# Optimization experiments

Hardware: AMD Instinct MI355X
Metric: run time of the kernel (lower is better)

## Reference

```python
import jax, jax.numpy as jnp
import numpy as np

EMB = 1024
HEADS = 16
HEAD_SZ = EMB // HEADS
EPS = 1e-5


def _layernorm(x, g, b):
    mu = jnp.mean(x, axis=-1, keepdims=True)
    var = jnp.mean(jnp.square(x - mu), axis=-1, keepdims=True)
    return (x - mu) * jax.lax.rsqrt(var + EPS) * g + b


def setup_inputs() -> dict:
    key = jax.random.key(0)
    ks = jax.random.split(key, 12)
    s_in = 1.0 / np.sqrt(EMB)
    s_h = 1.0 / np.sqrt(4 * EMB)
    return {
        "x": jax.random.normal(ks[0], (4, 1024, EMB), jnp.float32),
        # per-head Q/K/V projections stacked: [H, EMB, HEAD_SZ], no bias
        "wq": jax.random.normal(ks[1], (HEADS, EMB, HEAD_SZ), jnp.float32) * s_in,
        "wk": jax.random.normal(ks[2], (HEADS, EMB, HEAD_SZ), jnp.float32) * s_in,
        "wv": jax.random.normal(ks[3], (HEADS, EMB, HEAD_SZ), jnp.float32) * s_in,
        "w_proj": jax.random.normal(ks[4], (EMB, EMB), jnp.float32) * s_in,
        "b_proj": jnp.zeros((EMB,), jnp.float32),
        "w1": jax.random.normal(ks[5], (EMB, 4 * EMB), jnp.float32) * s_in,
        "b1": jnp.zeros((4 * EMB,), jnp.float32),
        "w2": jax.random.normal(ks[6], (4 * EMB, EMB), jnp.float32) * s_h,
        "b2": jnp.zeros((EMB,), jnp.float32),
        "g1": jnp.ones((EMB,), jnp.float32),
        "be1": jnp.zeros((EMB,), jnp.float32),
        "g2": jnp.ones((EMB,), jnp.float32),
        "be2": jnp.zeros((EMB,), jnp.float32),
    }


def reference(x, wq, wk, wv, w_proj, b_proj, w1, b1, w2, b2, g1, be1, g2, be2):
    B, T, C = x.shape
    # --- self-attention (pre-norm) ---
    h = _layernorm(x, g1, be1)
    q = jnp.einsum("btc,hcd->bhtd", h, wq)
    k = jnp.einsum("btc,hcd->bhtd", h, wk)
    v = jnp.einsum("btc,hcd->bhtd", h, wv)
    scale = 1.0 / jnp.sqrt(jnp.asarray(HEAD_SZ, x.dtype))
    scores = jnp.einsum("bhtd,bhsd->bhts", q, k) * scale  # non-causal: SDPA called with no mask
    attn = jax.nn.softmax(scores, axis=-1)
    o = jnp.einsum("bhts,bhsd->bhtd", attn, v)
    o = o.transpose(0, 2, 1, 3).reshape(B, T, C)  # concat heads (same order as torch.cat)
    sa_out = o @ w_proj + b_proj
    x = x + sa_out
    # --- feed-forward; note ln2 applied twice, faithful to source ---
    t = _layernorm(x, g2, be2)
    t = _layernorm(t, g2, be2)
    ff = jax.nn.relu(t @ w1 + b1) @ w2 + b2
    return x + ff
```

## Files before the change

### kernel.cpp

```cpp
#include <hip/hip_runtime.h>
#include <hip/hip_bf16.h>
#include <math.h>
#include <stdint.h>

typedef __bf16 bf16_t;
typedef __bf16 bf16x4 __attribute__((ext_vector_type(4)));
typedef __bf16 bf16x8 __attribute__((ext_vector_type(8)));
typedef float floatx4 __attribute__((ext_vector_type(4)));

#define BM 128
#define BK 32

__device__ __forceinline__ void gload16(const void* g, void* lds) {
    __builtin_amdgcn_global_load_lds(
        (__attribute__((address_space(1))) void*)(uintptr_t)g,
        (__attribute__((address_space(3))) void*)(uintptr_t)lds,
        16, 0, 0);
}

__global__ void transpose_all(const float* __restrict__ wq, const float* __restrict__ wk,
                              const float* __restrict__ wv, const float* __restrict__ w_proj,
                              const float* __restrict__ w1, const float* __restrict__ w2,
                              bf16_t* __restrict__ WQKVT, bf16_t* __restrict__ WPROJT,
                              bf16_t* __restrict__ W1T, bf16_t* __restrict__ W2T)
{
    const int idx = blockIdx.x;
    const float* in; bf16_t* out; int R, C, rt, ct; long nrow0;
    if (idx < 768) {
        const int z = idx >> 8;
        const int hd = (idx >> 4) & 15;
        rt = idx & 15; ct = 0; R = 1024; C = 64;
        in  = (z == 0 ? wq : z == 1 ? wk : wv) + hd * 65536;
        out = WQKVT; nrow0 = z * 1024 + hd * 64;
    } else if (idx < 1024) {
        const int t = idx - 768; rt = t & 15; ct = t >> 4; R = 1024; C = 1024;
        in = w_proj; out = WPROJT; nrow0 = 0;
    } else if (idx < 2048) {
        const int t = idx - 1024; rt = t & 15; ct = t >> 4; R = 1024; C = 4096;
        in = w1; out = W1T; nrow0 = 0;
    } else {
        const int t = idx - 2048; rt = t & 63; ct = t >> 6; R = 4096; C = 1024;
        in = w2; out = W2T; nrow0 = 0;
    }
    __shared__ float tile[64][65];
    const int tid = threadIdx.x;
    const int r0 = rt * 64, c0 = ct * 64;
    const int tr = tid >> 4;
    const int tc = (tid & 15) * 4;
#pragma unroll
    for (int rr = 0; rr < 4; rr++) {
        const int r = tr + rr * 16;
        const float4 v = *(const float4*)&in[(long)(r0 + r) * C + c0 + tc];
        tile[r][tc + 0] = v.x; tile[r][tc + 1] = v.y;
        tile[r][tc + 2] = v.z; tile[r][tc + 3] = v.w;
    }
    __syncthreads();
    const int KT = R >> 5;
#pragma unroll
    for (int rr = 0; rr < 4; rr++) {
        const int c = tr + rr * 16;
        const long n = nrow0 + c0 + c;
        const int k = r0 + tc;
        bf16x4 o;
        o[0] = (bf16_t)tile[tc + 0][c];
        o[1] = (bf16_t)tile[tc + 1][c];
        o[2] = (bf16_t)tile[tc + 2][c];
        o[3] = (bf16_t)tile[tc + 3][c];
        const long addr = ((n >> 4) * KT + (k >> 5)) * 512
                        + (((k >> 3) & 3) * 16 + (n & 15)) * 8 + (k & 7);
        *(bf16x4*)&out[addr] = o;
    }
}

__global__ void ln_kernel(const float* __restrict__ x, const float* __restrict__ g,
                          const float* __restrict__ b, bf16_t* __restrict__ outb)
{
    const int row = blockIdx.x;
    const int tid = threadIdx.x;
    const float4 v = ((const float4*)(x + (long)row * 1024))[tid];
    float s  = v.x + v.y + v.z + v.w;
    float s2 = v.x * v.x + v.y * v.y + v.z * v.z + v.w * v.w;
#pragma unroll
    for (int off = 32; off >= 1; off >>= 1) {
        s  += __shfl_xor(s, off);
        s2 += __shfl_xor(s2, off);
    }
    __shared__ float red[8];
    const int wv = tid >> 6;
    if ((tid & 63) == 0) { red[wv] = s; red[4 + wv] = s2; }
    __syncthreads();
    s  = red[0] + red[1] + red[2] + red[3];
    s2 = red[4] + red[5] + red[6] + red[7];
    const float mu  = s * (1.0f / 1024.0f);
    const float var = fmaxf(s2 * (1.0f / 1024.0f) - mu * mu, 0.0f);
    const float rs  = rsqrtf(var + 1e-5f);
    const float4 gv = ((const float4*)g)[tid];
    const float4 bv = ((const float4*)b)[tid];
    bf16x4 o;
    o[0] = (bf16_t)((v.x - mu) * rs * gv.x + bv.x);
    o[1] = (bf16_t)((v.y - mu) * rs * gv.y + bv.y);
    o[2] = (bf16_t)((v.z - mu) * rs * gv.z + bv.z);
    o[3] = (bf16_t)((v.w - mu) * rs * gv.w + bv.w);
    ((bf16x4*)(outb + (long)row * 1024))[tid] = o;
}

__global__ void ln2x_kernel(const float* __restrict__ x, const float* __restrict__ g,
                            const float* __restrict__ b, bf16_t* __restrict__ outb)
{
    const int row = blockIdx.x;
    const int tid = threadIdx.x;
    const float4 v = ((const float4*)(x + (long)row * 1024))[tid];
    float s  = v.x + v.y + v.z + v.w;
    float s2 = v.x * v.x + v.y * v.y + v.z * v.z + v.w * v.w;
#pragma unroll
    for (int off = 32; off >= 1; off >>= 1) {
        s  += __shfl_xor(s, off);
        s2 += __shfl_xor(s2, off);
    }
    __shared__ float red[8];
    __shared__ float red2[8];
    const int wv = tid >> 6;
    if ((tid & 63) == 0) { red[wv] = s; red[4 + wv] = s2; }
    __syncthreads();
    s  = red[0] + red[1] + red[2] + red[3];
    s2 = red[4] + red[5] + red[6] + red[7];
    float mu  = s * (1.0f / 1024.0f);
    float var = fmaxf(s2 * (1.0f / 1024.0f) - mu * mu, 0.0f);
    float rs  = rsqrtf(var + 1e-5f);
    const float4 gv = ((const float4*)g)[tid];
    const float4 bv = ((const float4*)b)[tid];
    float y0 = (v.x - mu) * rs * gv.x + bv.x;
    float y1 = (v.y - mu) * rs * gv.y + bv.y;
    float y2 = (v.z - mu) * rs * gv.z + bv.z;
    float y3 = (v.w - mu) * rs * gv.w + bv.w;
    s  = y0 + y1 + y2 + y3;
    s2 = y0 * y0 + y1 * y1 + y2 * y2 + y3 * y3;
#pragma unroll
    for (int off = 32; off >= 1; off >>= 1) {
        s  += __shfl_xor(s, off);
        s2 += __shfl_xor(s2, off);
    }
    if ((tid & 63) == 0) { red2[wv] = s; red2[4 + wv] = s2; }
    __syncthreads();
    s  = red2[0] + red2[1] + red2[2] + red2[3];
    s2 = red2[4] + red2[5] + red2[6] + red2[7];
    mu  = s * (1.0f / 1024.0f);
    var = fmaxf(s2 * (1.0f / 1024.0f) - mu * mu, 0.0f);
    rs  = rsqrtf(var + 1e-5f);
    bf16x4 o;
    o[0] = (bf16_t)((y0 - mu) * rs * gv.x + bv.x);
    o[1] = (bf16_t)((y1 - mu) * rs * gv.y + bv.y);
    o[2] = (bf16_t)((y2 - mu) * rs * gv.z + bv.z);
    o[3] = (bf16_t)((y3 - mu) * rs * gv.w + bv.w);
    ((bf16x4*)(outb + (long)row * 1024))[tid] = o;
}

template<int EPI, int BNt>
__global__ __launch_bounds__(256, 2)
void gemm_bt(const bf16_t* __restrict__ A, const bf16_t* __restrict__ Bt,
             const int K,
             const float* __restrict__ bias, const float* __restrict__ resid,
             float* __restrict__ outf, bf16_t* __restrict__ outb,
             bf16_t* __restrict__ aux1, bf16_t* __restrict__ aux2,
             const int Nout)
{
    constexpr int NFRAG = BNt / 16;
    __shared__ __align__(16) bf16_t As[3][BM * BK];
    __shared__ __align__(16) bf16_t Bs[3][NFRAG * 512];
    const int tid  = threadIdx.x;
    const int wave = tid >> 6, lane = tid & 63;
    const int bm = blockIdx.x * BM, bn = blockIdx.y * BNt;

    floatx4 acc[2][NFRAG];
#pragma unroll
    for (int i = 0; i < 2; i++)
#pragma unroll
        for (int j = 0; j < NFRAG; j++) acc[i][j] = (floatx4){0.f, 0.f, 0.f, 0.f};

    const int srow  = lane >> 2;
    const int selem = (lane & 3) * 8;
    const bf16_t* gA0 = A + (size_t)(bm + wave * 32 + srow) * K + selem;
    const bf16_t* gA1 = gA0 + (size_t)16 * K;
    const int laOff0 = (wave * 32 + srow) * BK + selem;
    const int laOff1 = laOff0 + 16 * BK;
    const int lA0 = (wave * 32) * BK;
    const int lA1 = (wave * 32 + 16) * BK;

    const int KT = K >> 5;
    const bf16_t* gB0;
    const bf16_t* gB1 = nullptr;
    int lB0, lB1 = 0;
    if (BNt == 128) {
        gB0 = Bt + ((size_t)(bn / 16 + wave * 2 + 0) * KT) * 512 + lane * 8;
        gB1 = Bt + ((size_t)(bn / 16 + wave * 2 + 1) * KT) * 512 + lane * 8;
        lB0 = (wave * 2 + 0) * 512;
        lB1 = (wave * 2 + 1) * 512;
    } else {
        gB0 = Bt + ((size_t)(bn / 16 + wave) * KT) * 512 + lane * 8;
        lB0 = wave * 512;
    }

    const int fr = lane & 15;
    const int fk = (lane >> 4) * 8;

    auto stage = [&](int t, int bu) {
        const size_t offA = (size_t)t * BK;
        const size_t offB = (size_t)t * 512;
        gload16(gA0 + offA, (bf16_t*)As[bu] + lA0);
        gload16(gA1 + offA, (bf16_t*)As[bu] + lA1);
        gload16(gB0 + offB, (bf16_t*)Bs[bu] + lB0);
        if (BNt == 128) gload16(gB1 + offB, (bf16_t*)Bs[bu] + lB1);
    };

    auto compute = [&](int bu) {
        bf16x8 af[2], bfv[NFRAG];
#pragma unroll
        for (int i = 0; i < 2; i++)
            af[i] = *(const bf16x8*)&As[bu][(wave * 32 + i * 16 + fr) * BK + fk];
#pragma unroll
        for (int j = 0; j < NFRAG; j++)
            bfv[j] = *(const bf16x8*)&Bs[bu][j * 512 + lane * 8];
#pragma unroll
        for (int i = 0; i < 2; i++)
#pragma unroll
            for (int j = 0; j < NFRAG; j++)
                acc[i][j] = __builtin_amdgcn_mfma_f32_16x16x32_bf16(af[i], bfv[j], acc[i][j], 0, 0, 0);
    };

    const int NT = K / BK;
    stage(0, 0);
    stage(1, 1);
    int bu = 0;
    for (int t = 0; t < NT - 1; ++t) {
        if (BNt == 128) asm volatile("s_waitcnt vmcnt(4)\n\ts_barrier" ::: "memory");
        else            asm volatile("s_waitcnt vmcnt(3)\n\ts_barrier" ::: "memory");
        if (t + 2 < NT) stage(t + 2, (t + 2) % 3);
        compute(bu);
        bu = (bu + 1) % 3;
    }
    asm volatile("s_waitcnt vmcnt(0)\n\ts_barrier" ::: "memory");
    compute(bu);

    const int er = (lane >> 4) * 4, ec = lane & 15;
#pragma unroll
    for (int i = 0; i < 2; i++) {
#pragma unroll
        for (int j = 0; j < NFRAG; j++) {
            const int col = bn + j * 16 + ec;
#pragma unroll
            for (int r = 0; r < 4; r++) {
                const int row = bm + wave * 32 + i * 16 + er + r;
                const float v = acc[i][j][r];
                if (EPI == 0) {
                    const int b = row >> 10, t = row & 1023;
                    if (col < 1024) {
                        const int h = col >> 6, d = col & 63;
                        outb[(size_t)((b * 16 + h) * 1024 + t) * 64 + d] = (bf16_t)v;
                    } else if (col < 2048) {
                        const int c2 = col - 1024, h = c2 >> 6, d = c2 & 63;
                        aux1[(size_t)((b * 16 + h) * 1024 + t) * 64 + d] = (bf16_t)v;
                    } else {
                        const int c2 = col - 2048, h = c2 >> 6, d = c2 & 63;
                        aux2[(size_t)((b * 16 + h) * 64 + d) * 1024 + t] = (bf16_t)v;
                    }
                } else if (EPI == 1 || EPI == 3) {
                    const size_t idx = (size_t)row * Nout + col;
                    outf[idx] = v + bias[col] + resid[idx];
                } else if (EPI == 2) {
                    const size_t idx = (size_t)row * Nout + col;
                    outb[idx] = (bf16_t)fmaxf(v + bias[col], 0.f);
                }
            }
        }
    }
}

__global__ __launch_bounds__(256, 4)
void attn_kernel(const bf16_t* __restrict__ Q, const bf16_t* __restrict__ Kg,
                 const bf16_t* __restrict__ Vt, bf16_t* __restrict__ Og)
{
    __shared__ __align__(16) bf16_t Ks[2][4096];
    __shared__ __align__(16) bf16_t Vs[2][4096];
    __shared__ __align__(16) bf16_t Ps[4][1024];
    const int tid = threadIdx.x, wave = tid >> 6, lane = tid & 63;
    const int bh = blockIdx.y;
    const int b = bh >> 4, h = bh & 15;
    const int q0 = blockIdx.x * 64 + wave * 16;
    const bf16_t* Qb = Q + (size_t)bh * 65536;
    const char* Kb = (const char*)(Kg + (size_t)bh * 65536);
    const char* Vb = (const char*)(Vt + (size_t)bh * 65536);
    const int fr = lane & 15, g = lane >> 4, fk = g * 8;

    const bf16x8 qf0 = *(const bf16x8*)&Qb[(size_t)(q0 + fr) * 64 + fk];
    const bf16x8 qf1 = *(const bf16x8*)&Qb[(size_t)(q0 + fr) * 64 + 32 + fk];

    floatx4 o[4];
#pragma unroll
    for (int dt = 0; dt < 4; dt++) o[dt] = (floatx4){0.f, 0.f, 0.f, 0.f};
    float lsum[4] = {0.f, 0.f, 0.f, 0.f};
    bf16_t* pw = &Ps[wave][0];
    const float sscale = 0.125f * 1.44269504088896f;

    auto stage = [&](int s0, int bu) {
#pragma unroll
        for (int t = 0; t < 2; t++) {
            const int j = wave * 2 + t;
            gload16(Kb + (size_t)(s0 + lane) * 128 + j * 16, &Ks[bu][j * 512]);
            gload16(Vb + (size_t)lane * 2048 + (size_t)s0 * 2 + j * 16, &Vs[bu][j * 512]);
        }
    };

    stage(0, 0);
    int bu = 0;
    for (int it = 0; it < 16; ++it) {
        __syncthreads();
        if (it < 15) stage((it + 1) * 64, bu ^ 1);
        const bf16_t* Kl = Ks[bu];
        const bf16_t* Vl = Vs[bu];

        floatx4 sacc[4];
#pragma unroll
        for (int ss = 0; ss < 4; ss++) sacc[ss] = (floatx4){0.f, 0.f, 0.f, 0.f};
#pragma unroll
        for (int c = 0; c < 2; c++) {
            const int ch = c * 4 + g;
            const bf16x8 qf = (c == 0) ? qf0 : qf1;
#pragma unroll
            for (int ss = 0; ss < 4; ss++) {
                const bf16x8 kf = *(const bf16x8*)&Kl[ch * 512 + (ss * 16 + fr) * 8];
                sacc[ss] = __builtin_amdgcn_mfma_f32_16x16x32_bf16(qf, kf, sacc[ss], 0, 0, 0);
            }
        }
#pragma unroll
        for (int ss = 0; ss < 4; ss++) {
#pragma unroll
            for (int r = 0; r < 4; r++) {
                const float p = __builtin_amdgcn_exp2f(sacc[ss][r] * sscale);
                lsum[r] += p;
                const int q = g * 4 + r;
                pw[(ss * 2 + (fr >> 3)) * 128 + q * 8 + (fr & 7)] = (bf16_t)p;
            }
        }
        asm volatile("s_waitcnt lgkmcnt(0)" ::: "memory");
#pragma unroll
        for (int c = 0; c < 2; c++) {
            const int ch = c * 4 + g;
            const bf16x8 pf = *(const bf16x8*)&pw[ch * 128 + fr * 8];
#pragma unroll
            for (int dt = 0; dt < 4; dt++) {
                const bf16x8 vf = *(const bf16x8*)&Vl[ch * 512 + (dt * 16 + fr) * 8];
                o[dt] = __builtin_amdgcn_mfma_f32_16x16x32_bf16(pf, vf, o[dt], 0, 0, 0);
            }
        }
        asm volatile("" ::: "memory");
        bu ^= 1;
    }
#pragma unroll
    for (int r = 0; r < 4; r++) {
        float l = lsum[r];
        l += __shfl_xor(l, 1);
        l += __shfl_xor(l, 2);
        l += __shfl_xor(l, 4);
        l += __shfl_xor(l, 8);
        lsum[r] = 1.0f / l;
    }
    const int t = q0 + g * 4;
#pragma unroll
    for (int dt = 0; dt < 4; dt++) {
#pragma unroll
        for (int r = 0; r < 4; r++) {
            const size_t idx = ((size_t)(b * 1024 + t + r)) * 1024 + h * 64 + dt * 16 + fr;
            Og[idx] = (bf16_t)(o[dt][r] * lsum[r]);
        }
    }
}

extern "C" void kernel_launch(void* const* d_in, const int* in_sizes, int n_in,
                              void* d_out, int out_size, void* d_ws, size_t ws_size,
                              hipStream_t stream)
{
    const float* x      = (const float*)d_in[0];
    const float* wq     = (const float*)d_in[1];
    const float* wk     = (const float*)d_in[2];
    const float* wv     = (const float*)d_in[3];
    const float* w_proj = (const float*)d_in[4];
    const float* b_proj = (const float*)d_in[5];
    const float* w1     = (const float*)d_in[6];
    const float* b1     = (const float*)d_in[7];
    const float* w2     = (const float*)d_in[8];
    const float* b2     = (const float*)d_in[9];
    const float* g1     = (const float*)d_in[10];
    const float* be1    = (const float*)d_in[11];
    const float* g2     = (const float*)d_in[12];
    const float* be2    = (const float*)d_in[13];
    float* out = (float*)d_out;
    char* ws = (char*)d_ws;

    bf16_t* WQKVT = (bf16_t*)(ws + 0x0000000);
    bf16_t* WPROJT= (bf16_t*)(ws + 0x0600000);
    bf16_t* W1T   = (bf16_t*)(ws + 0x0800000);
    bf16_t* W2T   = (bf16_t*)(ws + 0x1000000);
    bf16_t* HB    = (bf16_t*)(ws + 0x1800000);
    bf16_t* Qb    = (bf16_t*)(ws + 0x2000000);
    bf16_t* Kb    = (bf16_t*)(ws + 0x2800000);
    bf16_t* Vtb   = (bf16_t*)(ws + 0x3000000);
    bf16_t* AO    = (bf16_t*)(ws + 0x3800000);
    float*  X2    = (float*)(ws + 0x4000000);
    bf16_t* TB    = (bf16_t*)(ws + 0x2800000);
    bf16_t* FF1B  = (bf16_t*)(ws + 0x5000000);

    dim3 blk(256);
    transpose_all<<<3072, blk, 0, stream>>>(wq, wk, wv, w_proj, w1, w2,
                                            WQKVT, WPROJT, W1T, W2T);
    ln_kernel<<<4096, blk, 0, stream>>>(x, g1, be1, HB);
    gemm_bt<0, 128><<<dim3(32, 24), blk, 0, stream>>>(HB, WQKVT, 1024, nullptr, nullptr,
                                                      nullptr, Qb, Kb, Vtb, 3072);
    attn_kernel<<<dim3(16, 64), blk, 0, stream>>>(Qb, Kb, Vtb, AO);
    gemm_bt<1, 64><<<dim3(32, 16), blk, 0, stream>>>(AO, WPROJT, 1024, b_proj, x,
                                                     X2, nullptr, nullptr, nullptr, 1024);
    ln2x_kernel<<<4096, blk, 0, stream>>>(X2, g2, be2, TB);
    gemm_bt<2, 128><<<dim3(32, 32), blk, 0, stream>>>(TB, W1T, 1024, b1, nullptr,
                                                      nullptr, FF1B, nullptr, nullptr, 4096);
    gemm_bt<3, 64><<<dim3(32, 16), blk, 0, stream>>>(FF1B, W2T, 4096, b2, X2,
                                                     out, nullptr, nullptr, nullptr, 1024);
}
```

Baseline: 308.9 us.

## Store GEMM A operands in pre-tiled fragment layout for contiguous LDS staging

Producers of GEMM A operands (layernorm kernels, attention output, FFN1 ReLU epilogue) now write activations in the same 16x32 fragment-tiled layout already used for transposed weights. The GEMM then loads A tiles as contiguous 1 KB chunks per wave and reads fragments linearly from LDS, as it already does for B. This targets strided global loads and possible LDS bank conflicts on the A side. In exchange the producer stores become more scattered, especially the per-element bf16 stores in the attention and FFN1 epilogues.

```diff
diff --git a/kernel.cpp b/kernel.cpp
--- a/kernel.cpp
+++ b/kernel.cpp
@@ -10,6 +10,11 @@
 
 #define BM 128
 #define BK 32
+
+__device__ __forceinline__ size_t ftaddr(int m, int k, int KT) {
+    return ((size_t)(m >> 4) * KT + (k >> 5)) * 512
+         + (((k >> 3) & 3) * 16 + (m & 15)) * 8 + (k & 7);
+}
 
 __device__ __forceinline__ void gload16(const void* g, void* lds) {
     __builtin_amdgcn_global_load_lds(
@@ -66,9 +71,7 @@
         o[1] = (bf16_t)tile[tc + 1][c];
         o[2] = (bf16_t)tile[tc + 2][c];
         o[3] = (bf16_t)tile[tc + 3][c];
-        const long addr = ((n >> 4) * KT + (k >> 5)) * 512
-                        + (((k >> 3) & 3) * 16 + (n & 15)) * 8 + (k & 7);
-        *(bf16x4*)&out[addr] = o;
+        *(bf16x4*)&out[ftaddr((int)n, k, KT)] = o;
     }
 }
 
@@ -101,7 +104,7 @@
     o[1] = (bf16_t)((v.y - mu) * rs * gv.y + bv.y);
     o[2] = (bf16_t)((v.z - mu) * rs * gv.z + bv.z);
     o[3] = (bf16_t)((v.w - mu) * rs * gv.w + bv.w);
-    ((bf16x4*)(outb + (long)row * 1024))[tid] = o;
+    *(bf16x4*)&outb[ftaddr(row, tid * 4, 32)] = o;
 }
 
 __global__ void ln2x_kernel(const float* __restrict__ x, const float* __restrict__ g,
@@ -152,7 +155,7 @@
     o[1] = (bf16_t)((y1 - mu) * rs * gv.y + bv.y);
     o[2] = (bf16_t)((y2 - mu) * rs * gv.z + bv.z);
     o[3] = (bf16_t)((y3 - mu) * rs * gv.w + bv.w);
-    ((bf16x4*)(outb + (long)row * 1024))[tid] = o;
+    *(bf16x4*)&outb[ftaddr(row, tid * 4, 32)] = o;
 }
 
 template<int EPI, int BNt>
@@ -165,11 +168,12 @@
              const int Nout)
 {
     constexpr int NFRAG = BNt / 16;
-    __shared__ __align__(16) bf16_t As[3][BM * BK];
+    __shared__ __align__(16) bf16_t As[3][8 * 512];
     __shared__ __align__(16) bf16_t Bs[3][NFRAG * 512];
     const int tid  = threadIdx.x;
     const int wave = tid >> 6, lane = tid & 63;
     const int bm = blockIdx.x * BM, bn = blockIdx.y * BNt;
+    const int KT = K >> 5;
 
     floatx4 acc[2][NFRAG];
 #pragma unroll
@@ -177,16 +181,11 @@
 #pragma unroll
         for (int j = 0; j < NFRAG; j++) acc[i][j] = (floatx4){0.f, 0.f, 0.f, 0.f};
 
-    const int srow  = lane >> 2;
-    const int selem = (lane & 3) * 8;
-    const bf16_t* gA0 = A + (size_t)(bm + wave * 32 + srow) * K + selem;
-    const bf16_t* gA1 = gA0 + (size_t)16 * K;
-    const int laOff0 = (wave * 32 + srow) * BK + selem;
-    const int laOff1 = laOff0 + 16 * BK;
-    const int lA0 = (wave * 32) * BK;
-    const int lA1 = (wave * 32 + 16) * BK;
-
-    const int KT = K >> 5;
+    const bf16_t* gA0 = A + ((size_t)(bm / 16 + wave * 2 + 0) * KT) * 512 + lane * 8;
+    const bf16_t* gA1 = A + ((size_t)(bm / 16 + wave * 2 + 1) * KT) * 512 + lane * 8;
+    const int lA0 = (wave * 2 + 0) * 512;
+    const int lA1 = (wave * 2 + 1) * 512;
+
     const bf16_t* gB0;
     const bf16_t* gB1 = nullptr;
     int lB0, lB1 = 0;
@@ -200,23 +199,19 @@
         lB0 = wave * 512;
     }
 
-    const int fr = lane & 15;
-    const int fk = (lane >> 4) * 8;
-
     auto stage = [&](int t, int bu) {
-        const size_t offA = (size_t)t * BK;
-        const size_t offB = (size_t)t * 512;
-        gload16(gA0 + offA, (bf16_t*)As[bu] + lA0);
-        gload16(gA1 + offA, (bf16_t*)As[bu] + lA1);
-        gload16(gB0 + offB, (bf16_t*)Bs[bu] + lB0);
-        if (BNt == 128) gload16(gB1 + offB, (bf16_t*)Bs[bu] + lB1);
+        const size_t off = (size_t)t * 512;
+        gload16(gA0 + off, (bf16_t*)As[bu] + lA0);
+        gload16(gA1 + off, (bf16_t*)As[bu] + lA1);
+        gload16(gB0 + off, (bf16_t*)Bs[bu] + lB0);
+        if (BNt == 128) gload16(gB1 + off, (bf16_t*)Bs[bu] + lB1);
     };
 
     auto compute = [&](int bu) {
         bf16x8 af[2], bfv[NFRAG];
 #pragma unroll
         for (int i = 0; i < 2; i++)
-            af[i] = *(const bf16x8*)&As[bu][(wave * 32 + i * 16 + fr) * BK + fk];
+            af[i] = *(const bf16x8*)&As[bu][(wave * 2 + i) * 512 + lane * 8];
 #pragma unroll
         for (int j = 0; j < NFRAG; j++)
             bfv[j] = *(const bf16x8*)&Bs[bu][j * 512 + lane * 8];
@@ -267,8 +262,7 @@
                     const size_t idx = (size_t)row * Nout + col;
                     outf[idx] = v + bias[col] + resid[idx];
                 } else if (EPI == 2) {
-                    const size_t idx = (size_t)row * Nout + col;
-                    outb[idx] = (bf16_t)fmaxf(v + bias[col], 0.f);
+                    outb[ftaddr(row, col, Nout >> 5)] = (bf16_t)fmaxf(v + bias[col], 0.f);
                 }
             }
         }
@@ -364,13 +358,14 @@
         l += __shfl_xor(l, 8);
         lsum[r] = 1.0f / l;
     }
-    const int t = q0 + g * 4;
+    const int tq = q0 + g * 4;
 #pragma unroll
     for (int dt = 0; dt < 4; dt++) {
 #pragma unroll
         for (int r = 0; r < 4; r++) {
-            const size_t idx = ((size_t)(b * 1024 + t + r)) * 1024 + h * 64 + dt * 16 + fr;
-            Og[idx] = (bf16_t)(o[dt][r] * lsum[r]);
+            const int m = b * 1024 + tq + r;
+            const int k = h * 64 + dt * 16 + fr;
+            Og[ftaddr(m, k, 32)] = (bf16_t)(o[dt][r] * lsum[r]);
         }
     }
 }
```

Measured after the change: 318.9 us. +3.3%, slower.
